# Kernel optimization log

Measured on AMD Instinct MI355X. Metric: run time of the kernel, lower is better.

The kernel has to match this reference:

```python
import jax, jax.numpy as jnp
import numpy as np

EMBED = 1024
HEADS = 16
HEAD_DIM = EMBED // HEADS


def setup_inputs() -> dict:
    key = jax.random.key(0)
    ks = jax.random.split(key, 12)
    B, S = 2, 2048
    inp = {
        "query": jax.random.normal(ks[0], (B, S, EMBED), dtype=jnp.float32),
        "key": jax.random.normal(ks[1], (B, S, EMBED), dtype=jnp.float32),
        "value": jax.random.normal(ks[2], (B, S, EMBED), dtype=jnp.float32),
        "mask": jnp.ones((B, 1, 1, S), dtype=jnp.int32),
    }
    scale = 1.0 / np.sqrt(EMBED)
    inp["Wq"] = jax.random.normal(ks[3], (EMBED, EMBED), dtype=jnp.float32) * scale
    inp["bq"] = jax.random.normal(ks[4], (EMBED,), dtype=jnp.float32) * 0.01
    inp["Wk"] = jax.random.normal(ks[5], (EMBED, EMBED), dtype=jnp.float32) * scale
    inp["bk"] = jax.random.normal(ks[6], (EMBED,), dtype=jnp.float32) * 0.01
    inp["Wv"] = jax.random.normal(ks[7], (EMBED, EMBED), dtype=jnp.float32) * scale
    inp["bv"] = jax.random.normal(ks[8], (EMBED,), dtype=jnp.float32) * 0.01
    inp["Wo"] = jax.random.normal(ks[9], (EMBED, EMBED), dtype=jnp.float32) * scale
    inp["bo"] = jax.random.normal(ks[10], (EMBED,), dtype=jnp.float32) * 0.01
    return inp


def reference(query, key, value, mask, Wq, bq, Wk, bk, Wv, bv, Wo, bo):
    N, Lq, _ = query.shape
    Lk = key.shape[1]
    # Linear projections (torch Linear: x @ W.T + b)
    q = (query @ Wq.T + bq).reshape(N, Lq, HEADS, HEAD_DIM)
    k = (key @ Wk.T + bk).reshape(N, Lk, HEADS, HEAD_DIM)
    v = (value @ Wv.T + bv).reshape(N, Lk, HEADS, HEAD_DIM)
    # scores: [N, H, Lq, Lk]
    energy = jnp.einsum("nqhd,nkhd->nhqk", q, k)
    energy = jnp.where(mask == 0, jnp.float32(-1e20), energy)
    # NOTE: original scales by sqrt(embedSize), not sqrt(head_dim)
    attn = jax.nn.softmax(energy / jnp.sqrt(jnp.float32(EMBED)), axis=3)
    out = jnp.einsum("nhqv,nvhd->nqhd", attn, v).reshape(N, Lq, EMBED)
    return out @ Wo.T + bo
```

## Files before the change

### kernel.cpp

```cpp
#include <hip/hip_runtime.h>
#include <stdint.h>

typedef unsigned short u16;
typedef __attribute__((ext_vector_type(8))) short short8;
typedef __attribute__((ext_vector_type(4))) short short4v;
typedef __attribute__((ext_vector_type(4))) float floatx4;
typedef __attribute__((ext_vector_type(16))) float floatx16;
typedef __attribute__((ext_vector_type(2))) unsigned int uint2v;
typedef __attribute__((ext_vector_type(4))) unsigned int uint4v;

#define AS_GLOBAL __attribute__((address_space(1)))
#define AS_LDS    __attribute__((address_space(3)))

#define QSCALE 0.045084220f

__device__ __forceinline__ float bf2f(u16 u) {
  union { unsigned int i; float f; } x; x.i = ((unsigned int)u) << 16; return x.f;
}
__device__ __forceinline__ u16 f2bf(float f) {
  union { float f; unsigned int i; } x; x.f = f;
  unsigned int u = x.i;
  u += 0x7fffu + ((u >> 16) & 1u);
  return (u16)(u >> 16);
}
__device__ __forceinline__ u16 f2bf_fast(float f) {
  union { float f; unsigned int i; } x; x.f = f;
  return (u16)((x.i + 0x8000u) >> 16);
}

__device__ __forceinline__ unsigned int cvtpk_bf16(float lo, float hi) {
  unsigned int w;
  __asm__("v_cvt_pk_bf16_f32 %0, %1, %2" : "=v"(w) : "v"(lo), "v"(hi));
  return w;
}

__device__ __forceinline__ void pl32_swap(unsigned int& a, unsigned int& b) {
#if __has_builtin(__builtin_amdgcn_permlane32_swap)
  uint2v r = __builtin_amdgcn_permlane32_swap(a, b, false, false);
  a = r[0]; b = r[1];
#else
  __asm__("v_permlane32_swap_b32 %0, %1" : "+v"(a), "+v"(b));
#endif
}

__device__ __forceinline__ int probe_is_f32(const void* p) {
  const unsigned int* w = (const unsigned int*)p;
  int cnt = 0;
#pragma unroll
  for (int i = 0; i < 64; ++i) {
    unsigned int lo = w[i] & 0xFFFFu;
    int e = (int)((lo >> 7) & 0xFFu);
    cnt += (e >= 117 && e <= 137) ? 1 : 0;
  }
  return cnt < 32;
}

__device__ __forceinline__ short8 ld8(const void* P, size_t off, int isf32) {
  if (isf32) {
    const float* q = (const float*)P + off;
    float4 x = *(const float4*)q;
    float4 y = *(const float4*)(q + 4);
    short8 r;
    r[0] = (short)f2bf(x.x); r[1] = (short)f2bf(x.y);
    r[2] = (short)f2bf(x.z); r[3] = (short)f2bf(x.w);
    r[4] = (short)f2bf(y.x); r[5] = (short)f2bf(y.y);
    r[6] = (short)f2bf(y.z); r[7] = (short)f2bf(y.w);
    return r;
  }
  return *(const short8*)((const u16*)P + off);
}

__device__ __forceinline__ float ldscalar(const void* P, size_t idx, int isf32) {
  return isf32 ? ((const float*)P)[idx] : bf2f(((const u16*)P)[idx]);
}

__global__ __launch_bounds__(256) void cvt7(
    const void* s0, const void* s1, const void* s2, const void* s3,
    const void* s4, const void* s5, const void* s6,
    u16* d0, u16* d1, u16* d2, u16* d3, u16* d4, u16* d5, u16* d6)
{
  const int z = blockIdx.y;
  const void* src; u16* dst; int n;
  switch (z) {
    case 0: src = s0; dst = d0; n = 4194304; break;
    case 1: src = s1; dst = d1; n = 4194304; break;
    case 2: src = s2; dst = d2; n = 4194304; break;
    case 3: src = s3; dst = d3; n = 1048576; break;
    case 4: src = s4; dst = d4; n = 1048576; break;
    case 5: src = s5; dst = d5; n = 1048576; break;
    default: src = s6; dst = d6; n = 1048576; break;
  }
  const int isf32 = probe_is_f32(src);
  for (int i = blockIdx.x * 256 + threadIdx.x; i * 4 < n; i += gridDim.x * 256) {
    if (isf32) {
      float4 x = ((const float4*)src)[i];
      short4v r;
      r[0] = (short)f2bf(x.x); r[1] = (short)f2bf(x.y);
      r[2] = (short)f2bf(x.z); r[3] = (short)f2bf(x.w);
      *(short4v*)(dst + (size_t)i * 4) = r;
    } else {
      *(short4v*)(dst + (size_t)i * 4) = ((const short4v*)src)[i];
    }
  }
}

__device__ __forceinline__ void gemm_core_bf16_n64(
    const u16* __restrict__ A, const u16* __restrict__ W,
    u16* As, u16* Bs, floatx4 acc[2][4], int m0, int n0, int K, int tid)
{
  const int lane = tid & 63, wv = tid >> 6;
  const int g = lane >> 4, ml = lane & 15;
  const int r0 = tid >> 2, kc = (tid & 3) << 3;
  const u16* Ag0 = A + (size_t)(m0 + r0) * K + kc;
  const u16* Ag1 = A + (size_t)(m0 + r0 + 64) * K + kc;
  const u16* Bg0 = W + (size_t)(n0 + r0) * K + kc;

#define STAGE_N64(buf_, kt_) do {                                              \
    u16* a0 = As + (buf_) * 4096 + tid * 8;                                    \
    u16* b0 = Bs + (buf_) * 2048 + tid * 8;                                    \
    __builtin_amdgcn_global_load_lds((const AS_GLOBAL unsigned int*)(Ag0 + (kt_)), \
                                     (AS_LDS unsigned int*)a0, 16, 0, 0);      \
    __builtin_amdgcn_global_load_lds((const AS_GLOBAL unsigned int*)(Ag1 + (kt_)), \
                                     (AS_LDS unsigned int*)(a0 + 2048), 16, 0, 0); \
    __builtin_amdgcn_global_load_lds((const AS_GLOBAL unsigned int*)(Bg0 + (kt_)), \
                                     (AS_LDS unsigned int*)b0, 16, 0, 0);      \
  } while (0)

  STAGE_N64(0, 0);
  int buf = 0;
#pragma unroll 2
  for (int kt = 0; kt < K; kt += 32) {
    const int nk = (kt + 32 < K) ? (kt + 32) : 0;
    STAGE_N64(buf ^ 1, nk);
    __asm__ __volatile__("s_waitcnt vmcnt(3)\n\ts_barrier" ::: "memory");
    const u16* Ac = As + buf * 4096;
    const u16* Bc = Bs + buf * 2048;
    short8 af[2], bf[4];
#pragma unroll
    for (int i = 0; i < 2; ++i)
      af[i] = *(const short8*)(Ac + (wv * 32 + i * 16 + ml) * 32 + g * 8);
#pragma unroll
    for (int j = 0; j < 4; ++j)
      bf[j] = *(const short8*)(Bc + (j * 16 + ml) * 32 + g * 8);
#pragma unroll
    for (int i = 0; i < 2; ++i)
#pragma unroll
      for (int j = 0; j < 4; ++j)
        acc[i][j] = __builtin_amdgcn_mfma_f32_16x16x32_bf16(af[i], bf[j], acc[i][j], 0, 0, 0);
    __asm__ __volatile__("s_waitcnt lgkmcnt(0)\n\ts_barrier" ::: "memory");
    buf ^= 1;
  }
#undef STAGE_N64
  __asm__ __volatile__("s_waitcnt vmcnt(0)" ::: "memory");
}

__device__ __forceinline__ void gemm_core_cvt(
    const void* __restrict__ A, const void* __restrict__ W, int aF32, int bF32,
    u16* As, u16* Bs, floatx4 acc[4][4], int m0, int n0, int K, int tid)
{
  const int lane = tid & 63, wv = tid >> 6;
  const int wm = wv >> 1, wn = wv & 1;
  const int g = lane >> 4, ml = lane & 15;
  const int r0 = tid >> 2, kc = (tid & 3) << 3;
  const size_t offA0 = (size_t)(m0 + r0) * K + kc;
  const size_t offA1 = (size_t)(m0 + r0 + 64) * K + kc;
  const size_t offB0 = (size_t)(n0 + r0) * K + kc;
  const size_t offB1 = (size_t)(n0 + r0 + 64) * K + kc;
  u16* Al0 = As + tid * 8;  u16* Al1 = As + (tid + 256) * 8;
  u16* Bl0 = Bs + tid * 8;  u16* Bl1 = Bs + (tid + 256) * 8;
  for (int kt = 0; kt < K; kt += 32) {
    short8 a0 = ld8(A, offA0 + kt, aF32);
    short8 a1 = ld8(A, offA1 + kt, aF32);
    short8 b0 = ld8(W, offB0 + kt, bF32);
    short8 b1 = ld8(W, offB1 + kt, bF32);
    *(short8*)Al0 = a0;  *(short8*)Al1 = a1;
    *(short8*)Bl0 = b0;  *(short8*)Bl1 = b1;
    __syncthreads();
    short8 af[4], bf[4];
#pragma unroll
    for (int i = 0; i < 4; ++i)
      af[i] = *(const short8*)(As + (wm * 64 + i * 16 + ml) * 32 + g * 8);
#pragma unroll
    for (int j = 0; j < 4; ++j)
      bf[j] = *(const short8*)(Bs + (wn * 64 + j * 16 + ml) * 32 + g * 8);
#pragma unroll
    for (int i = 0; i < 4; ++i)
#pragma unroll
      for (int j = 0; j < 4; ++j)
        acc[i][j] = __builtin_amdgcn_mfma_f32_16x16x32_bf16(af[i], bf[j], acc[i][j], 0, 0, 0);
    __syncthreads();
  }
}

__device__ __forceinline__ void qkv_epilogue64(
    floatx4 acc[2][4], const void* Bi, int cF32, u16* O, int m0, int n0,
    int tid, int z)
{
  const int lane = tid & 63, wv = tid >> 6;
  const int g = lane >> 4, ml = lane & 15;
  const float sc = (z == 0) ? QSCALE : 1.0f;
#pragma unroll
  for (int j = 0; j < 4; ++j) {
    int gn = n0 + j * 16 + ml;
    float bvv = ldscalar(Bi, (size_t)gn, cF32);
    int h = gn >> 6, d = gn & 63;
    if (z == 2) {
#pragma unroll
      for (int i = 0; i < 2; ++i) {
        int gm0 = m0 + wv * 32 + i * 16 + g * 4;
        int b = gm0 >> 11, s0 = gm0 & 2047;
        short4v pk;
#pragma unroll
        for (int r = 0; r < 4; ++r) pk[r] = (short)f2bf_fast(acc[i][j][r] + bvv);
        *(short4v*)(O + ((((size_t)b * 16 + h) * 64 + d) * 2048 + s0)) = pk;
      }
    } else {
#pragma unroll
      for (int i = 0; i < 2; ++i)
#pragma unroll
        for (int r = 0; r < 4; ++r) {
          int gm = m0 + wv * 32 + i * 16 + g * 4 + r;
          int b = gm >> 11, s = gm & 2047;
          O[(((size_t)b * 16 + h) * 2048 + s) * 64 + d] =
              f2bf_fast((acc[i][j][r] + bvv) * sc);
        }
    }
  }
}

__device__ __forceinline__ void qkv_epilogue(
    floatx4 acc[4][4], const void* Bi, int cF32, u16* O, int m0, int n0,
    int tid, int z)
{
  const int lane = tid & 63, wv = tid >> 6;
  const int wm = wv >> 1, wn = wv & 1, g = lane >> 4, ml = lane & 15;
  const float sc = (z == 0) ? QSCALE : 1.0f;
#pragma unroll
  for (int j = 0; j < 4; ++j) {
    int gn = n0 + wn * 64 + j * 16 + ml;
    float bvv = ldscalar(Bi, (size_t)gn, cF32);
    int h = gn >> 6, d = gn & 63;
    if (z == 2) {
#pragma unroll
      for (int i = 0; i < 4; ++i) {
        int gm0 = m0 + wm * 64 + i * 16 + g * 4;
        int b = gm0 >> 11, s0 = gm0 & 2047;
        short4v pk;
#pragma unroll
        for (int r = 0; r < 4; ++r) pk[r] = (short)f2bf_fast(acc[i][j][r] + bvv);
        *(short4v*)(O + ((((size_t)b * 16 + h) * 64 + d) * 2048 + s0)) = pk;
      }
    } else {
#pragma unroll
      for (int i = 0; i < 4; ++i)
#pragma unroll
        for (int r = 0; r < 4; ++r) {
          int gm = m0 + wm * 64 + i * 16 + g * 4 + r;
          int b = gm >> 11, s = gm & 2047;
          O[(((size_t)b * 16 + h) * 2048 + s) * 64 + d] =
              f2bf_fast((acc[i][j][r] + bvv) * sc);
        }
    }
  }
}

__global__ __launch_bounds__(256, 6) void qkv_gemm_bf16(
    const u16* __restrict__ Xq, const u16* __restrict__ Xk, const u16* __restrict__ Xv,
    const u16* __restrict__ Wq, const u16* __restrict__ Wk, const u16* __restrict__ Wv,
    const void* __restrict__ Bq, const void* __restrict__ Bk, const void* __restrict__ Bv,
    u16* __restrict__ Oq, u16* __restrict__ Ok, u16* __restrict__ Ov)
{
  __align__(16) __shared__ u16 As[8192];
  __align__(16) __shared__ u16 Bs[4096];
  const int z = blockIdx.z;
  const u16* X = (z == 0) ? Xq : (z == 1) ? Xk : Xv;
  const u16* W = (z == 0) ? Wq : (z == 1) ? Wk : Wv;
  const void* Bi = (z == 0) ? Bq : (z == 1) ? Bk : Bv;
  u16* O = (z == 0) ? Oq : (z == 1) ? Ok : Ov;
  const int tid = threadIdx.x;
  const int m0 = blockIdx.x * 128, n0 = blockIdx.y * 64;
  floatx4 acc[2][4] = {};
  gemm_core_bf16_n64(X, W, As, Bs, acc, m0, n0, 1024, tid);
  const int cF32 = probe_is_f32(Bi);
  qkv_epilogue64(acc, Bi, cF32, O, m0, n0, tid, z);
}

__global__ __launch_bounds__(256) void qkv_gemm_cvt(
    const void* __restrict__ Xq, const void* __restrict__ Xk, const void* __restrict__ Xv,
    const void* __restrict__ Wq, const void* __restrict__ Wk, const void* __restrict__ Wv,
    const void* __restrict__ Bq, const void* __restrict__ Bk, const void* __restrict__ Bv,
    u16* __restrict__ Oq, u16* __restrict__ Ok, u16* __restrict__ Ov)
{
  __align__(16) __shared__ u16 As[4096];
  __align__(16) __shared__ u16 Bs[4096];
  const int z = blockIdx.z;
  const void* X  = (z == 0) ? Xq : (z == 1) ? Xk : Xv;
  const void* W  = (z == 0) ? Wq : (z == 1) ? Wk : Wv;
  const void* Bi = (z == 0) ? Bq : (z == 1) ? Bk : Bv;
  u16* O = (z == 0) ? Oq : (z == 1) ? Ok : Ov;
  const int aF32 = probe_is_f32(X);
  const int bF32 = probe_is_f32(W);
  const int cF32 = probe_is_f32(Bi);
  const int tid = threadIdx.x;
  const int m0 = blockIdx.y * 128, n0 = blockIdx.x * 128;
  floatx4 acc[4][4] = {};
  gemm_core_cvt(X, W, aF32, bF32, As, Bs, acc, m0, n0, 1024, tid);
  qkv_epilogue(acc, Bi, cF32, O, m0, n0, tid, z);
}

__global__ __launch_bounds__(256, 6) void out_gemm_bf16(
    const u16* __restrict__ X, const u16* __restrict__ W,
    const void* __restrict__ Bi, float* __restrict__ O)
{
  __align__(16) __shared__ u16 As[8192];
  __align__(16) __shared__ u16 Bs[4096];
  const int tid = threadIdx.x;
  const int m0 = blockIdx.x * 128, n0 = blockIdx.y * 64;
  floatx4 acc[2][4] = {};
  gemm_core_bf16_n64(X, W, As, Bs, acc, m0, n0, 1024, tid);
  const int cF32 = probe_is_f32(Bi);
  const int lane = tid & 63, wv = tid >> 6;
  const int g = lane >> 4, ml = lane & 15;
#pragma unroll
  for (int j = 0; j < 4; ++j) {
    int gn = n0 + j * 16 + ml;
    float bvv = ldscalar(Bi, (size_t)gn, cF32);
#pragma unroll
    for (int i = 0; i < 2; ++i)
#pragma unroll
      for (int r = 0; r < 4; ++r) {
        int gm = m0 + wv * 32 + i * 16 + g * 4 + r;
        O[(size_t)gm * 1024 + gn] = acc[i][j][r] + bvv;
      }
  }
}

__global__ __launch_bounds__(256) void out_gemm_cvt(
    const u16* __restrict__ X, const void* __restrict__ W,
    const void* __restrict__ Bi, float* __restrict__ O)
{
  __align__(16) __shared__ u16 As[4096];
  __align__(16) __shared__ u16 Bs[4096];
  const int bF32 = probe_is_f32(W);
  const int cF32 = probe_is_f32(Bi);
  const int tid = threadIdx.x;
  const int m0 = blockIdx.y * 128, n0 = blockIdx.x * 128;
  floatx4 acc[4][4] = {};
  gemm_core_cvt(X, W, 0, bF32, As, Bs, acc, m0, n0, 1024, tid);
  const int lane = tid & 63, wv = tid >> 6;
  const int wm = wv >> 1, wn = wv & 1, g = lane >> 4, ml = lane & 15;
#pragma unroll
  for (int j = 0; j < 4; ++j) {
    int gn = n0 + wn * 64 + j * 16 + ml;
    float bvv = ldscalar(Bi, (size_t)gn, cF32);
#pragma unroll
    for (int i = 0; i < 4; ++i)
#pragma unroll
      for (int r = 0; r < 4; ++r) {
        int gm = m0 + wm * 64 + i * 16 + g * 4 + r;
        O[(size_t)gm * 1024 + gn] = acc[i][j][r] + bvv;
      }
  }
}

__global__ __launch_bounds__(256, 4) void flash_attn(
    const u16* __restrict__ Q, const u16* __restrict__ K, const u16* __restrict__ V,
    const int* __restrict__ Mask, u16* __restrict__ O)
{
  __align__(16) __shared__ u16 Ks[2][64 * 64];
  __align__(16) __shared__ u16 Vt[2][64 * 64];
  __align__(16) __shared__ int Ms[64];
  __align__(16) __shared__ float Lf[256];
  __shared__ int Wok[4];

  const int wgid = blockIdx.x + (blockIdx.y << 5);
  const int swz  = ((wgid & 7) << 7) | (wgid >> 3);
  const int qt = swz & 31;
  const int bh = swz >> 5;
  const int b = bh >> 4, h = bh & 15;
  const int tid = threadIdx.x;
  const int lane = tid & 63, wv = tid >> 6;
  const int qh = wv & 1, kh = wv >> 1;
  const int H = lane >> 5, lq = lane & 31;
  const int koff = lq * 16 + H * 8;

  const size_t baseQ  = (((size_t)b * 16 + h) * 2048 + (size_t)qt * 64) * 64;
  const size_t baseKV = ((size_t)b * 16 + h) * 2048 * 64;

  {
    int la = 1;
#pragma unroll
    for (int i = 0; i < 8; ++i) la &= Mask[b * 2048 + tid * 8 + i];
    int wall = __all(la != 0);
    if (lane == 0) Wok[wv] = wall;
  }

  short8 qf[4];
  {
    const u16* qb = Q + baseQ + (size_t)(qh * 32 + lq) * 64 + H * 8;
#pragma unroll
    for (int c = 0; c < 4; ++c)
      qf[c] = *(const short8*)(qb + c * 16);
  }

  const u16* kg[2]; const u16* vg[2];
  int lo[2];
#pragma unroll
  for (int t = 0; t < 2; ++t) {
    int s = tid + t * 256;
    int blk = s >> 8;
    int ch  = (s >> 6) & 3;
    int row = (s >> 1) & 31;
    int hh  = s & 1;
    kg[t] = K + baseKV + (size_t)(blk * 32 + row) * 64 + ch * 16 + hh * 8;
    vg[t] = V + baseKV + (size_t)(blk * 32 + row) * 2048 + ch * 16 + hh * 8;
    lo[t] = ((tid & 192) + t * 256) * 8;
  }

#pragma unroll
  for (int t = 0; t < 2; ++t) {
    __builtin_amdgcn_global_load_lds((const AS_GLOBAL unsigned int*)kg[t],
                                     (AS_LDS unsigned int*)(&Ks[0][0] + lo[t]), 16, 0, 0);
    __builtin_amdgcn_global_load_lds((const AS_GLOBAL unsigned int*)vg[t],
                                     (AS_LDS unsigned int*)(&Vt[0][0] + lo[t]), 16, 0, 0);
  }

  __syncthreads();
  const bool maskall = Wok[0] && Wok[1] && Wok[2] && Wok[3];

  floatx16 oacc0 = {}, oacc1 = {};
  float lp = 0.f;

  int buf = 0;
#pragma unroll 2
  for (int kv0 = 0; kv0 < 2048; kv0 += 64) {
    const int nxt = (kv0 + 64) & 2047;
#pragma unroll
    for (int t = 0; t < 2; ++t) {
      __builtin_amdgcn_global_load_lds((const AS_GLOBAL unsigned int*)(vg[t] + nxt),
                                       (AS_LDS unsigned int*)(&Vt[buf ^ 1][0] + lo[t]), 16, 0, 0);
      __builtin_amdgcn_global_load_lds((const AS_GLOBAL unsigned int*)(kg[t] + (size_t)nxt * 64),
                                       (AS_LDS unsigned int*)(&Ks[buf ^ 1][0] + lo[t]), 16, 0, 0);
    }
    if (!maskall && tid < 64) Ms[tid] = Mask[b * 2048 + kv0 + tid];
    __asm__ __volatile__("s_waitcnt vmcnt(4) lgkmcnt(0)\n\ts_barrier" ::: "memory");

    const u16* Kc = &Ks[buf][0];
    floatx16 a = {};
    __builtin_amdgcn_s_setprio(1);
#pragma unroll
    for (int c = 0; c < 4; ++c) {
      short8 kb = *(const short8*)(Kc + (kh * 4 + c) * 512 + koff);
      a = __builtin_amdgcn_mfma_f32_32x32x16_bf16(kb, qf[c], a, 0, 0, 0);
    }
    __builtin_amdgcn_s_setprio(0);

    float sv[16];
#pragma unroll
    for (int r = 0; r < 16; ++r) sv[r] = a[r];
    if (!maskall) {
#pragma unroll
      for (int r = 0; r < 16; ++r) {
        int ko = 32 * kh + (r & 3) + 8 * (r >> 2) + 4 * H;
        if (Ms[ko] == 0) sv[r] = -1.0e30f;
      }
    }
#pragma unroll
    for (int r = 0; r < 16; ++r) {
      float p = __builtin_amdgcn_exp2f(sv[r]);
      sv[r] = p;
      lp += p;
    }

    unsigned int Wd[8];
#pragma unroll
    for (int i = 0; i < 8; ++i)
      Wd[i] = cvtpk_bf16(sv[2 * i], sv[2 * i + 1]);
    short8 pa[2];
#define MAKE_PA(dst_, Wsrc_, base_) do {                                       \
    unsigned int u0 = Wsrc_[base_],       u1 = Wsrc_[(base_) + 1];             \
    unsigned int v0 = Wsrc_[(base_) + 2], v1 = Wsrc_[(base_) + 3];             \
    pl32_swap(u0, v0); pl32_swap(u1, v1);                                      \
    uint4v pw; pw[0] = u0; pw[1] = u1; pw[2] = v0; pw[3] = v1;                 \
    dst_ = __builtin_bit_cast(short8, pw);                                     \
  } while (0)
    MAKE_PA(pa[0], Wd, 0);
    MAKE_PA(pa[1], Wd, 4);
#undef MAKE_PA

    const u16* Vc = &Vt[buf][0];
    __builtin_amdgcn_s_setprio(1);
#pragma unroll
    for (int c = 0; c < 2; ++c) {
      short8 vb = *(const short8*)(Vc + (2 * kh + c) * 512 + koff);
      oacc0 = __builtin_amdgcn_mfma_f32_32x32x16_bf16(pa[c], vb, oacc0, 0, 0, 0);
    }
#pragma unroll
    for (int c = 0; c < 2; ++c) {
      short8 vb = *(const short8*)(Vc + (4 + 2 * kh + c) * 512 + koff);
      oacc1 = __builtin_amdgcn_mfma_f32_32x32x16_bf16(pa[c], vb, oacc1, 0, 0, 0);
    }
    __builtin_amdgcn_s_setprio(0);

    __asm__ __volatile__("s_barrier" ::: "memory");
    buf ^= 1;
  }
  __asm__ __volatile__("s_waitcnt vmcnt(0)" ::: "memory");
  __syncthreads();

  float lh = lp + __shfl_xor(lp, 32);
  Lf[wv * 64 + lane] = lh;
  float* Xf = (float*)&Ks[0][0];
  {
    float* myreg = Xf + wv * 1024;
    const floatx16& dep = kh ? oacc0 : oacc1;
#pragma unroll
    for (int w = 0; w < 4; ++w) {
      float4 f4;
      f4.x = dep[4 * w + 0]; f4.y = dep[4 * w + 1];
      f4.z = dep[4 * w + 2]; f4.w = dep[4 * w + 3];
      *(float4*)(myreg + w * 256 + lane * 4) = f4;
    }
  }
  __syncthreads();
  const int pwv = wv ^ 2;
  float l = lh + Lf[pwv * 64 + lane];
  float inv = (l > 0.f) ? 1.0f / l : 0.f;
  floatx16 mine = kh ? oacc1 : oacc0;
  {
    const float* prr = Xf + pwv * 1024;
#pragma unroll
    for (int w = 0; w < 4; ++w) {
      float4 f4 = *(const float4*)(prr + w * 256 + lane * 4);
      mine[4 * w + 0] += f4.x; mine[4 * w + 1] += f4.y;
      mine[4 * w + 2] += f4.z; mine[4 * w + 3] += f4.w;
    }
  }

#pragma unroll
  for (int r = 0; r < 16; ++r) {
    int qo = (r & 3) + 8 * (r >> 2) + 4 * H;
    float ivr = __shfl(inv, qo);
    int q = qt * 64 + qh * 32 + qo;
    size_t orow = ((size_t)b * 2048 + q) * 1024 + (size_t)h * 64;
    O[orow + kh * 32 + lq] = f2bf_fast(mine[r] * ivr);
  }
}

extern "C" void kernel_launch(void* const* d_in, const int* in_sizes, int n_in,
                              void* d_out, int out_size, void* d_ws, size_t ws_size,
                              hipStream_t stream) {
  const void* q_in = d_in[0];
  const void* k_in = d_in[1];
  const void* v_in = d_in[2];
  const int* mask = (const int*)d_in[3];
  const void* Wq = d_in[4];  const void* bq = d_in[5];
  const void* Wk = d_in[6];  const void* bk = d_in[7];
  const void* Wv = d_in[8];  const void* bv = d_in[9];
  const void* Wo = d_in[10]; const void* bo = d_in[11];

  const size_t NTOK = (size_t)2 * 2048 * 1024;
  const size_t NW   = (size_t)1024 * 1024;

  if (ws_size >= (size_t)67108864) {
    u16* CXq = (u16*)d_ws;
    u16* CXk = CXq + NTOK;
    u16* CXv = CXk + NTOK;
    u16* CWq = CXv + NTOK;
    u16* CWk = CWq + NW;
    u16* CWv = CWk + NW;
    u16* CWo = CWv + NW;
    u16* Qp  = CWo + NW;
    u16* Kp  = Qp + NTOK;
    u16* Vp  = Kp + NTOK;
    u16* Ao  = Vp + NTOK;

    cvt7<<<dim3(1024, 7), 256, 0, stream>>>(q_in, k_in, v_in, Wq, Wk, Wv, Wo,
                                            CXq, CXk, CXv, CWq, CWk, CWv, CWo);
    qkv_gemm_bf16<<<dim3(32, 16, 3), 256, 0, stream>>>(CXq, CXk, CXv,
                                                       CWq, CWk, CWv,
                                                       bq, bk, bv, Qp, Kp, Vp);
    flash_attn<<<dim3(32, 32), 256, 0, stream>>>(Qp, Kp, Vp, mask, Ao);
    out_gemm_bf16<<<dim3(32, 16), 256, 0, stream>>>(Ao, CWo, bo, (float*)d_out);
  } else {
    u16* Qp = (u16*)d_ws;
    u16* Kp = Qp + NTOK;
    u16* Vp = Kp + NTOK;
    u16* Ao  = Vp + NTOK;

    qkv_gemm_cvt<<<dim3(8, 32, 3), 256, 0, stream>>>(q_in, k_in, v_in,
                                                     Wq, Wk, Wv, bq, bk, bv,
                                                     Qp, Kp, Vp);
    flash_attn<<<dim3(32, 32), 256, 0, stream>>>(Qp, Kp, Vp, mask, Ao);
    out_gemm_cvt<<<dim3(8, 32), 256, 0, stream>>>(Ao, Wo, bo, (float*)d_out);
  }
}
```

Measured before the change: 235.2 us.

## Use 64x64 tiles for output GEMM and tweak attention loop address/sum math

Result: no change. 237.1 us (+0.8%).

```diff
diff --git a/kernel.cpp b/kernel.cpp
--- a/kernel.cpp
+++ b/kernel.cpp
@@ -151,6 +151,47 @@
     buf ^= 1;
   }
 #undef STAGE_N64
+  __asm__ __volatile__("s_waitcnt vmcnt(0)" ::: "memory");
+}
+
+__device__ __forceinline__ void gemm_core_bf16_6464(
+    const u16* __restrict__ A, const u16* __restrict__ W,
+    u16* As, u16* Bs, floatx4 acc[4], int m0, int n0, int K, int tid)
+{
+  const int lane = tid & 63, wv = tid >> 6;
+  const int g = lane >> 4, ml = lane & 15;
+  const int r0 = tid >> 2, kc = (tid & 3) << 3;
+  const u16* Ag = A + (size_t)(m0 + r0) * K + kc;
+  const u16* Bg = W + (size_t)(n0 + r0) * K + kc;
+
+#define STAGE_6464(buf_, kt_) do {                                             \
+    __builtin_amdgcn_global_load_lds((const AS_GLOBAL unsigned int*)(Ag + (kt_)), \
+        (AS_LDS unsigned int*)(As + (buf_) * 2048 + tid * 8), 16, 0, 0);       \
+    __builtin_amdgcn_global_load_lds((const AS_GLOBAL unsigned int*)(Bg + (kt_)), \
+        (AS_LDS unsigned int*)(Bs + (buf_) * 2048 + tid * 8), 16, 0, 0);       \
+  } while (0)
+
+  STAGE_6464(0, 0);
+  int buf = 0;
+#pragma unroll 2
+  for (int kt = 0; kt < K; kt += 32) {
+    const int nk = (kt + 32 < K) ? (kt + 32) : 0;
+    STAGE_6464(buf ^ 1, nk);
+    __asm__ __volatile__("s_waitcnt vmcnt(2)\n\ts_barrier" ::: "memory");
+    const u16* Ac = As + buf * 2048;
+    const u16* Bc = Bs + buf * 2048;
+    short8 af = *(const short8*)(Ac + (wv * 16 + ml) * 32 + g * 8);
+    short8 bf[4];
+#pragma unroll
+    for (int j = 0; j < 4; ++j)
+      bf[j] = *(const short8*)(Bc + (j * 16 + ml) * 32 + g * 8);
+#pragma unroll
+    for (int j = 0; j < 4; ++j)
+      acc[j] = __builtin_amdgcn_mfma_f32_16x16x32_bf16(af, bf[j], acc[j], 0, 0, 0);
+    __asm__ __volatile__("s_waitcnt lgkmcnt(0)\n\ts_barrier" ::: "memory");
+    buf ^= 1;
+  }
+#undef STAGE_6464
   __asm__ __volatile__("s_waitcnt vmcnt(0)" ::: "memory");
 }
 
@@ -308,16 +349,16 @@
   qkv_epilogue(acc, Bi, cF32, O, m0, n0, tid, z);
 }
 
-__global__ __launch_bounds__(256, 6) void out_gemm_bf16(
+__global__ __launch_bounds__(256, 4) void out_gemm_bf16(
     const u16* __restrict__ X, const u16* __restrict__ W,
     const void* __restrict__ Bi, float* __restrict__ O)
 {
-  __align__(16) __shared__ u16 As[8192];
+  __align__(16) __shared__ u16 As[4096];
   __align__(16) __shared__ u16 Bs[4096];
   const int tid = threadIdx.x;
-  const int m0 = blockIdx.x * 128, n0 = blockIdx.y * 64;
-  floatx4 acc[2][4] = {};
-  gemm_core_bf16_n64(X, W, As, Bs, acc, m0, n0, 1024, tid);
+  const int m0 = blockIdx.x * 64, n0 = blockIdx.y * 64;
+  floatx4 acc[4] = {};
+  gemm_core_bf16_6464(X, W, As, Bs, acc, m0, n0, 1024, tid);
   const int cF32 = probe_is_f32(Bi);
   const int lane = tid & 63, wv = tid >> 6;
   const int g = lane >> 4, ml = lane & 15;
@@ -326,12 +367,10 @@
     int gn = n0 + j * 16 + ml;
     float bvv = ldscalar(Bi, (size_t)gn, cF32);
 #pragma unroll
-    for (int i = 0; i < 2; ++i)
-#pragma unroll
-      for (int r = 0; r < 4; ++r) {
-        int gm = m0 + wv * 32 + i * 16 + g * 4 + r;
-        O[(size_t)gm * 1024 + gn] = acc[i][j][r] + bvv;
-      }
+    for (int r = 0; r < 4; ++r) {
+      int gm = m0 + wv * 16 + g * 4 + r;
+      O[(size_t)gm * 1024 + gn] = acc[j][r] + bvv;
+    }
   }
 }
 
@@ -404,6 +443,7 @@
   }
 
   const u16* kg[2]; const u16* vg[2];
+  const u16* kgp[2]; const u16* vgp[2];
   int lo[2];
 #pragma unroll
   for (int t = 0; t < 2; ++t) {
@@ -414,6 +454,8 @@
     int hh  = s & 1;
     kg[t] = K + baseKV + (size_t)(blk * 32 + row) * 64 + ch * 16 + hh * 8;
     vg[t] = V + baseKV + (size_t)(blk * 32 + row) * 2048 + ch * 16 + hh * 8;
+    kgp[t] = kg[t] + 4096;
+    vgp[t] = vg[t] + 64;
     lo[t] = ((tid & 192) + t * 256) * 8;
   }
 
@@ -429,18 +471,19 @@
   const bool maskall = Wok[0] && Wok[1] && Wok[2] && Wok[3];
 
   floatx16 oacc0 = {}, oacc1 = {};
-  float lp = 0.f;
+  float lp0 = 0.f, lp1 = 0.f, lp2 = 0.f, lp3 = 0.f;
 
   int buf = 0;
 #pragma unroll 2
   for (int kv0 = 0; kv0 < 2048; kv0 += 64) {
-    const int nxt = (kv0 + 64) & 2047;
 #pragma unroll
     for (int t = 0; t < 2; ++t) {
-      __builtin_amdgcn_global_load_lds((const AS_GLOBAL unsigned int*)(vg[t] + nxt),
+      __builtin_amdgcn_global_load_lds((const AS_GLOBAL unsigned int*)vgp[t],
                                        (AS_LDS unsigned int*)(&Vt[buf ^ 1][0] + lo[t]), 16, 0, 0);
-      __builtin_amdgcn_global_load_lds((const AS_GLOBAL unsigned int*)(kg[t] + (size_t)nxt * 64),
+      __builtin_amdgcn_global_load_lds((const AS_GLOBAL unsigned int*)kgp[t],
                                        (AS_LDS unsigned int*)(&Ks[buf ^ 1][0] + lo[t]), 16, 0, 0);
+      vgp[t] += 64;
+      kgp[t] += 4096;
     }
     if (!maskall && tid < 64) Ms[tid] = Mask[b * 2048 + kv0 + tid];
     __asm__ __volatile__("s_waitcnt vmcnt(4) lgkmcnt(0)\n\ts_barrier" ::: "memory");
@@ -469,7 +512,10 @@
     for (int r = 0; r < 16; ++r) {
       float p = __builtin_amdgcn_exp2f(sv[r]);
       sv[r] = p;
-      lp += p;
+      if ((r & 3) == 0)      lp0 += p;
+      else if ((r & 3) == 1) lp1 += p;
+      else if ((r & 3) == 2) lp2 += p;
+      else                   lp3 += p;
     }
 
     unsigned int Wd[8];
@@ -508,6 +554,8 @@
   __asm__ __volatile__("s_waitcnt vmcnt(0)" ::: "memory");
   __syncthreads();
 
+  const float lp = (lp0 + lp1) + (lp2 + lp3);
+
   float lh = lp + __shfl_xor(lp, 32);
   Lf[wv * 64 + lane] = lh;
   float* Xf = (float*)&Ks[0][0];
@@ -581,7 +629,7 @@
                                                        CWq, CWk, CWv,
                                                        bq, bk, bv, Qp, Kp, Vp);
     flash_attn<<<dim3(32, 32), 256, 0, stream>>>(Qp, Kp, Vp, mask, Ao);
-    out_gemm_bf16<<<dim3(32, 16), 256, 0, stream>>>(Ao, CWo, bo, (float*)d_out);
+    out_gemm_bf16<<<dim3(64, 16), 256, 0, stream>>>(Ao, CWo, bo, (float*)d_out);
   } else {
     u16* Qp = (u16*)d_ws;
     u16* Kp = Qp + NTOK;
```
